# Performance work log

Measured on AMD Instinct MI355X. Metric: run time of the kernel, lower is better.

The kernel has to match this reference:

```python
import jax, jax.numpy as jnp
import numpy as np

K = 2  # top-k experts per token


def setup_inputs() -> dict:
    key = jax.random.key(0)
    k1, k2, k3, k4 = jax.random.split(key, 4)
    B, S, D, E, O = 4, 2048, 1024, 8, 1024
    x = jax.random.normal(k1, (B, S, D), dtype=jnp.float32)
    # gate weight: zero-init in the module; use small random values so routing is nontrivial
    Wg = jax.random.normal(k2, (E, D), dtype=jnp.float32) * 0.02
    # experts: E independent Linear(D -> O) layers, stacked
    We = jax.random.normal(k3, (E, O, D), dtype=jnp.float32) * (1.0 / np.sqrt(D))
    be = jax.random.normal(k4, (E, O), dtype=jnp.float32) * 0.01
    return {"x": x, "Wg": Wg, "We": We, "be": be}


def reference(x, Wg, We, be):
    B, S, D = x.shape
    xt = x.reshape(-1, D)                                  # [T, D]
    gate_logits = xt @ Wg.T                                # [T, E]
    vals, sel = jax.lax.top_k(gate_logits, K)              # [T, K] each
    w = jax.nn.softmax(vals.astype(jnp.float32), axis=1).astype(xt.dtype)  # [T, K]
    # all-expert outputs (E small), then gather the selected ones per token
    y = jnp.einsum('td,eod->teo', xt, We) + be[None]       # [T, E, O]
    y_sel = jnp.take_along_axis(y, sel[:, :, None], axis=1)  # [T, K, O]
    out = jnp.einsum('tk,tko->to', w, y_sel)               # [T, O]
    return out.reshape(B, S, -1)
```

## Files before the change

kernel.cpp:

```cpp
#include <hip/hip_runtime.h>
#include <hip/hip_bf16.h>

#define T_NUM 8192
#define D_DIM 1024
#define O_DIM 1024
#define E_NUM 8
#define CAP   8192
#define BM 128
#define BN 128
#define BK 32

typedef float  f32x4  __attribute__((ext_vector_type(4)));
typedef __bf16 bf16x8 __attribute__((ext_vector_type(8)));

__device__ __forceinline__ void gld_lds16(const void* g, void* l) {
  __builtin_amdgcn_global_load_lds(
      (__attribute__((address_space(1))) void*)(void*)(g),
      (__attribute__((address_space(3))) void*)(l), 16, 0, 0);
}

__device__ __forceinline__ unsigned short f2bf(float f) {
  __hip_bfloat16 h = __float2bfloat16(f);
  return __builtin_bit_cast(unsigned short, h);
}

__global__ __launch_bounds__(256) void cvt_kernel(const float* __restrict__ in,
                                                  ushort* __restrict__ out, int n4) {
  int i = blockIdx.x * 256 + threadIdx.x;
  if (i >= n4) return;
  float4 v = ((const float4*)in)[i];
  ushort4 r;
  r.x = f2bf(v.x); r.y = f2bf(v.y); r.z = f2bf(v.z); r.w = f2bf(v.w);
  ((ushort4*)out)[i] = r;
}

__global__ __launch_bounds__(256) void gate_kernel(const float* __restrict__ x,
                                                   const float* __restrict__ Wg,
                                                   ushort* __restrict__ xb,
                                                   int* __restrict__ counts,
                                                   int* __restrict__ perm,
                                                   float* __restrict__ wgt) {
  __shared__ int   s_sel[64][2];
  __shared__ float s_w[64][2];
  __shared__ int   s_hist[E_NUM];
  __shared__ int   s_cursor[E_NUM];

  int tid  = threadIdx.x;
  int lane = tid & 63;
  int wv   = tid >> 6;
  if (tid < E_NUM) s_hist[tid] = 0;

  int t0 = blockIdx.x * 64;

  for (int it = 0; it < 16; ++it) {
    int tl = wv * 16 + it;
    int t  = t0 + tl;
    const float4* xv = (const float4*)(x + (long)t * D_DIM);
    ushort4* xo = (ushort4*)(xb + (long)t * D_DIM);

    float acc[E_NUM];
#pragma unroll
    for (int e = 0; e < E_NUM; ++e) acc[e] = 0.f;

#pragma unroll
    for (int i = 0; i < 4; ++i) {
      float4 xf = xv[lane + i * 64];
      ushort4 r;
      r.x = f2bf(xf.x); r.y = f2bf(xf.y); r.z = f2bf(xf.z); r.w = f2bf(xf.w);
      xo[lane + i * 64] = r;
#pragma unroll
      for (int e = 0; e < E_NUM; ++e) {
        const float4* wv4 = (const float4*)(Wg + e * D_DIM);
        float4 wf = wv4[lane + i * 64];
        acc[e] += xf.x * wf.x + xf.y * wf.y + xf.z * wf.z + xf.w * wf.w;
      }
    }

    float logit[E_NUM];
#pragma unroll
    for (int e = 0; e < E_NUM; ++e) {
      float v = acc[e];
      for (int off = 32; off > 0; off >>= 1) v += __shfl_down(v, off);
      logit[e] = v;
    }

    if (lane == 0) {
      int e0 = 0; float v0 = logit[0];
#pragma unroll
      for (int e = 1; e < E_NUM; ++e)
        if (logit[e] > v0) { v0 = logit[e]; e0 = e; }
      int e1 = -1; float v1 = -1e30f;
#pragma unroll
      for (int e = 0; e < E_NUM; ++e) {
        if (e == e0) continue;
        if (logit[e] > v1) { v1 = logit[e]; e1 = e; }
      }
      float ex  = expf(v1 - v0);
      float den = 1.f + ex;
      s_sel[tl][0] = e0; s_w[tl][0] = 1.f / den;
      s_sel[tl][1] = e1; s_w[tl][1] = ex / den;
    }
  }
  __syncthreads();

  if (tid < 128) {
    int e = s_sel[tid >> 1][tid & 1];
    atomicAdd(&s_hist[e], 1);
  }
  __syncthreads();

  if (tid < E_NUM) s_cursor[tid] = atomicAdd(&counts[tid], s_hist[tid]);
  __syncthreads();

  if (tid < 128) {
    int tl = tid >> 1, k = tid & 1;
    int e  = s_sel[tl][k];
    int pos = atomicAdd(&s_cursor[e], 1);
    perm[e * CAP + pos] = t0 + tl;
    wgt [e * CAP + pos] = s_w[tl][k];
  }
}

__global__ __launch_bounds__(256) void moe_gemm(const __hip_bfloat16* __restrict__ xb,
                                                const __hip_bfloat16* __restrict__ wb,
                                                const float* __restrict__ be,
                                                const int* __restrict__ counts,
                                                const int* __restrict__ perm,
                                                const float* __restrict__ wgt,
                                                float* __restrict__ out) {
  int bid = blockIdx.x;
  int e  = bid >> 9;
  int rt = (bid >> 3) & 63;
  int ct = bid & 7;
  int n = counts[e];
  if (rt * BM >= n) return;

  __shared__ __hip_bfloat16 lds_a[BM * BK];
  __shared__ __hip_bfloat16 lds_b[BN * BK];

  int tid  = threadIdx.x;
  int lane = tid & 63;
  int wid  = tid >> 6;
  int wm = wid >> 1, wn = wid & 1;

  int arow0 = (tid >> 2);
  int cg    = tid & 3;
  const int*   permE = perm + e * CAP;
  const float* wgtE  = wgt  + e * CAP;
  int slot0 = min(rt * BM + arow0,      n - 1);
  int slot1 = min(rt * BM + 64 + arow0, n - 1);
  long tok0 = permE[slot0];
  long tok1 = permE[slot1];
  const __hip_bfloat16* ga0 = xb + tok0 * D_DIM + cg * 8;
  const __hip_bfloat16* ga1 = xb + tok1 * D_DIM + cg * 8;
  const __hip_bfloat16* gb0 = wb + ((long)e * O_DIM + ct * BN + arow0) * D_DIM + cg * 8;
  const __hip_bfloat16* gb1 = gb0 + 64 * D_DIM;

  char* lA = (char*)lds_a;
  char* lB = (char*)lds_b;

  f32x4 acc[4][4];
#pragma unroll
  for (int m = 0; m < 4; ++m)
#pragma unroll
    for (int nn = 0; nn < 4; ++nn) acc[m][nn] = (f32x4){0.f, 0.f, 0.f, 0.f};

  int lr = lane & 15;
  int lk = (lane >> 4) * 8;

  for (int k0 = 0; k0 < D_DIM; k0 += BK) {
    __syncthreads();
    gld_lds16(ga0 + k0, lA +        wid * 1024);
    gld_lds16(ga1 + k0, lA + 4096 + wid * 1024);
    gld_lds16(gb0 + k0, lB +        wid * 1024);
    gld_lds16(gb1 + k0, lB + 4096 + wid * 1024);
    __syncthreads();

    bf16x8 af[4], bfr[4];
#pragma unroll
    for (int m = 0; m < 4; ++m)
      af[m] = *(const bf16x8*)(lds_a + (wm * 64 + m * 16 + lr) * BK + lk);
#pragma unroll
    for (int nn = 0; nn < 4; ++nn)
      bfr[nn] = *(const bf16x8*)(lds_b + (wn * 64 + nn * 16 + lr) * BK + lk);

#pragma unroll
    for (int m = 0; m < 4; ++m)
#pragma unroll
      for (int nn = 0; nn < 4; ++nn)
        acc[m][nn] = __builtin_amdgcn_mfma_f32_16x16x32_bf16(af[m], bfr[nn], acc[m][nn], 0, 0, 0);
  }

  int base_m = rt * BM + wm * 64;
  int base_n = ct * BN + wn * 64;
  const float* beE = be + e * O_DIM;
#pragma unroll
  for (int m = 0; m < 4; ++m) {
#pragma unroll
    for (int r = 0; r < 4; ++r) {
      int s = base_m + m * 16 + (lane >> 4) * 4 + r;
      if (s < n) {
        long t  = permE[s];
        float w = wgtE[s];
        float* orow = out + t * O_DIM;
#pragma unroll
        for (int nn = 0; nn < 4; ++nn) {
          int o = base_n + nn * 16 + (lane & 15);
          atomicAdd(&orow[o], w * (acc[m][nn][r] + beE[o]));
        }
      }
    }
  }
}

extern "C" void kernel_launch(void* const* d_in, const int* in_sizes, int n_in,
                              void* d_out, int out_size, void* d_ws, size_t ws_size,
                              hipStream_t stream) {
  const float* x  = (const float*)d_in[0];
  const float* Wg = (const float*)d_in[1];
  const float* We = (const float*)d_in[2];
  const float* be = (const float*)d_in[3];
  float* out = (float*)d_out;

  char* p = (char*)d_ws;
  __hip_bfloat16* xb = (__hip_bfloat16*)p;  p += (size_t)T_NUM * D_DIM * 2;
  __hip_bfloat16* wb = (__hip_bfloat16*)p;  p += (size_t)E_NUM * O_DIM * D_DIM * 2;
  int* counts = (int*)p;                    p += 256;
  int* perm   = (int*)p;                    p += (size_t)E_NUM * CAP * 4;
  float* wgt  = (float*)p;

  hipMemsetAsync(counts, 0, 256, stream);
  hipMemsetAsync(d_out, 0, (size_t)out_size * sizeof(float), stream);

  int n_w = E_NUM * O_DIM * D_DIM;
  cvt_kernel<<<n_w / 4 / 256, 256, 0, stream>>>(We, (ushort*)wb, n_w / 4);
  gate_kernel<<<T_NUM / 64, 256, 0, stream>>>(x, Wg, (ushort*)xb, counts, perm, wgt);
  moe_gemm<<<E_NUM * 64 * 8, 256, 0, stream>>>(xb, wb, be, counts, perm, wgt, out);
}
```

Measured before the change: 249.3 us.

## Enlarge MoE GEMM tiles to 256x256x64 with 512-thread blocks

Grows the grouped expert GEMM tile from 128x128 with BK=32 to 256x256 with BK=64. Blocks go from 256 to 512 threads, each wave computes a 128x64 sub-tile, and the loads and LDS indexing are reworked to match. Larger tiles raise arithmetic intensity, halve the number of K-loop barriers and reuse each gathered A row across more output columns. In exchange, LDS use rises to 64KB per block and each thread holds a 32-tile accumulator set, which can cut occupancy. The coarser tiles also waste more padded rows for experts whose token counts do not fill a tile.

```diff
diff --git a/kernel.cpp b/kernel.cpp
--- a/kernel.cpp
+++ b/kernel.cpp
@@ -6,9 +6,9 @@
 #define O_DIM 1024
 #define E_NUM 8
 #define CAP   8192
-#define BM 128
-#define BN 128
-#define BK 32
+#define BM 256
+#define BN 256
+#define BK 64
 
 typedef float  f32x4  __attribute__((ext_vector_type(4)));
 typedef __bf16 bf16x8 __attribute__((ext_vector_type(8)));
@@ -121,19 +121,19 @@
   }
 }
 
-__global__ __launch_bounds__(256) void moe_gemm(const __hip_bfloat16* __restrict__ xb,
-                                                const __hip_bfloat16* __restrict__ wb,
-                                                const float* __restrict__ be,
-                                                const int* __restrict__ counts,
-                                                const int* __restrict__ perm,
-                                                const float* __restrict__ wgt,
-                                                float* __restrict__ out) {
+__global__ __launch_bounds__(512, 2) void moe_gemm(const __hip_bfloat16* __restrict__ xb,
+                                                   const __hip_bfloat16* __restrict__ wb,
+                                                   const float* __restrict__ be,
+                                                   const int* __restrict__ counts,
+                                                   const int* __restrict__ perm,
+                                                   const float* __restrict__ wgt,
+                                                   float* __restrict__ out) {
   int bid = blockIdx.x;
-  int e  = bid >> 9;
-  int rt = (bid >> 3) & 63;
-  int ct = bid & 7;
+  int e  = bid >> 7;
+  int rt = (bid >> 2) & 31;
+  int ct = bid & 3;
   int n = counts[e];
-  if (rt * BM >= n) return;
+  if (n == 0 || rt * BM >= n) return;
 
   __shared__ __hip_bfloat16 lds_a[BM * BK];
   __shared__ __hip_bfloat16 lds_b[BN * BK];
@@ -141,27 +141,23 @@
   int tid  = threadIdx.x;
   int lane = tid & 63;
   int wid  = tid >> 6;
-  int wm = wid >> 1, wn = wid & 1;
-
-  int arow0 = (tid >> 2);
-  int cg    = tid & 3;
+  int wm = wid >> 2, wn = wid & 3;
+
+  int srow  = tid >> 3;
+  int slot8 = tid & 7;
   const int*   permE = perm + e * CAP;
   const float* wgtE  = wgt  + e * CAP;
-  int slot0 = min(rt * BM + arow0,      n - 1);
-  int slot1 = min(rt * BM + 64 + arow0, n - 1);
-  long tok0 = permE[slot0];
-  long tok1 = permE[slot1];
-  const __hip_bfloat16* ga0 = xb + tok0 * D_DIM + cg * 8;
-  const __hip_bfloat16* ga1 = xb + tok1 * D_DIM + cg * 8;
-  const __hip_bfloat16* gb0 = wb + ((long)e * O_DIM + ct * BN + arow0) * D_DIM + cg * 8;
-  const __hip_bfloat16* gb1 = gb0 + 64 * D_DIM;
-
-  char* lA = (char*)lds_a;
-  char* lB = (char*)lds_b;
-
-  f32x4 acc[4][4];
-#pragma unroll
-  for (int m = 0; m < 4; ++m)
+  long tokA[4];
+#pragma unroll
+  for (int r = 0; r < 4; ++r) {
+    int s = min(rt * BM + r * 64 + srow, n - 1);
+    tokA[r] = permE[s];
+  }
+  const __hip_bfloat16* gB = wb + ((long)e * O_DIM + ct * BN) * D_DIM;
+
+  f32x4 acc[8][4];
+#pragma unroll
+  for (int m = 0; m < 8; ++m)
 #pragma unroll
     for (int nn = 0; nn < 4; ++nn) acc[m][nn] = (f32x4){0.f, 0.f, 0.f, 0.f};
 
@@ -170,32 +166,38 @@
 
   for (int k0 = 0; k0 < D_DIM; k0 += BK) {
     __syncthreads();
-    gld_lds16(ga0 + k0, lA +        wid * 1024);
-    gld_lds16(ga1 + k0, lA + 4096 + wid * 1024);
-    gld_lds16(gb0 + k0, lB +        wid * 1024);
-    gld_lds16(gb1 + k0, lB + 4096 + wid * 1024);
+#pragma unroll
+    for (int r = 0; r < 4; ++r)
+      gld_lds16(xb + tokA[r] * D_DIM + k0 + slot8 * 8,
+                (char*)lds_a + r * 8192 + wid * 1024);
+#pragma unroll
+    for (int r = 0; r < 4; ++r)
+      gld_lds16(gB + (long)(r * 64 + srow) * D_DIM + k0 + slot8 * 8,
+                (char*)lds_b + r * 8192 + wid * 1024);
     __syncthreads();
 
-    bf16x8 af[4], bfr[4];
-#pragma unroll
-    for (int m = 0; m < 4; ++m)
-      af[m] = *(const bf16x8*)(lds_a + (wm * 64 + m * 16 + lr) * BK + lk);
-#pragma unroll
-    for (int nn = 0; nn < 4; ++nn)
-      bfr[nn] = *(const bf16x8*)(lds_b + (wn * 64 + nn * 16 + lr) * BK + lk);
-
-#pragma unroll
-    for (int m = 0; m < 4; ++m)
+#pragma unroll
+    for (int kk = 0; kk < 2; ++kk) {
+      bf16x8 af[8], bf[4];
+#pragma unroll
+      for (int m = 0; m < 8; ++m)
+        af[m] = *(const bf16x8*)(lds_a + (wm * 128 + m * 16 + lr) * BK + kk * 32 + lk);
 #pragma unroll
       for (int nn = 0; nn < 4; ++nn)
-        acc[m][nn] = __builtin_amdgcn_mfma_f32_16x16x32_bf16(af[m], bfr[nn], acc[m][nn], 0, 0, 0);
-  }
-
-  int base_m = rt * BM + wm * 64;
+        bf[nn] = *(const bf16x8*)(lds_b + (wn * 64 + nn * 16 + lr) * BK + kk * 32 + lk);
+#pragma unroll
+      for (int m = 0; m < 8; ++m)
+#pragma unroll
+        for (int nn = 0; nn < 4; ++nn)
+          acc[m][nn] = __builtin_amdgcn_mfma_f32_16x16x32_bf16(af[m], bf[nn], acc[m][nn], 0, 0, 0);
+    }
+  }
+
+  int base_m = rt * BM + wm * 128;
   int base_n = ct * BN + wn * 64;
   const float* beE = be + e * O_DIM;
 #pragma unroll
-  for (int m = 0; m < 4; ++m) {
+  for (int m = 0; m < 8; ++m) {
 #pragma unroll
     for (int r = 0; r < 4; ++r) {
       int s = base_m + m * 16 + (lane >> 4) * 4 + r;
@@ -235,5 +237,5 @@
   int n_w = E_NUM * O_DIM * D_DIM;
   cvt_kernel<<<n_w / 4 / 256, 256, 0, stream>>>(We, (ushort*)wb, n_w / 4);
   gate_kernel<<<T_NUM / 64, 256, 0, stream>>>(x, Wg, (ushort*)xb, counts, perm, wgt);
-  moe_gemm<<<E_NUM * 64 * 8, 256, 0, stream>>>(xb, wb, be, counts, perm, wgt, out);
-}
+  moe_gemm<<<E_NUM * 32 * 4, 512, 0, stream>>>(xb, wb, be, counts, perm, wgt, out);
+}
```

Measured after the change: 302.5 us. 21.3% more time.
